# Optimization experiments

Measured on AMD Instinct MI355X. Metric: run time of the kernel, lower is better.

The kernel has to match this reference:

```python
import math
import jax, jax.numpy as jnp
import numpy as np

B, S, D, H = 4, 1024, 512, 8
DH = D // H  # 64
SQRT_DIM = math.sqrt(D)


def _relative_shift(pos_score):
    # pos_score: [B, H, S, S]
    b, h, s1, s2 = pos_score.shape
    zeros = jnp.zeros((b, h, s1, 1), dtype=pos_score.dtype)
    padded = jnp.concatenate([zeros, pos_score], axis=-1)      # [B,H,S,S+1]
    padded = padded.reshape(b, h, s2 + 1, s1)                  # [B,H,S+1,S]
    return padded[:, :, 1:].reshape(b, h, s1, s2)


def setup_inputs() -> dict:
    key = jax.random.key(0)
    ks = jax.random.split(key, 14)
    std = 0.02
    inp = {
        "query": jax.random.normal(ks[0], (B, S, D), jnp.float32),
        "key": jax.random.normal(ks[1], (B, S, D), jnp.float32),
        "value": jax.random.normal(ks[2], (B, S, D), jnp.float32),
        "pos_embedding": jax.random.normal(ks[3], (B, S, D), jnp.float32),
        # projection weights stored [in, out] so y = x @ W + b
        "Wq": jax.random.normal(ks[4], (D, D), jnp.float32) * std,
        "bq": jnp.zeros((D,), jnp.float32),
        "Wk": jax.random.normal(ks[5], (D, D), jnp.float32) * std,
        "bk": jnp.zeros((D,), jnp.float32),
        "Wv": jax.random.normal(ks[6], (D, D), jnp.float32) * std,
        "bv": jnp.zeros((D,), jnp.float32),
        "Wp": jax.random.normal(ks[7], (D, D), jnp.float32) * std,  # pos_proj, no bias
        "Wo": jax.random.normal(ks[8], (D, D), jnp.float32) * std,
        "bo": jnp.zeros((D,), jnp.float32),
        "u_bias": jax.random.normal(ks[9], (H, DH), jnp.float32) * std,
        "v_bias": jax.random.normal(ks[10], (H, DH), jnp.float32) * std,
    }
    return inp


def reference(query, key, value, pos_embedding, Wq, bq, Wk, bk, Wv, bv, Wp, Wo, bo, u_bias, v_bias):
    b = query.shape[0]
    q = (query @ Wq + bq).reshape(b, -1, H, DH)          # [B,S,H,DH]
    k = (key @ Wk + bk).reshape(b, -1, H, DH)            # [B,T,H,DH]
    v = (value @ Wv + bv).reshape(b, -1, H, DH)          # [B,T,H,DH]
    p = (pos_embedding @ Wp).reshape(b, -1, H, DH)       # [B,T,H,DH]

    # content score: (q + u) . k  -> [B,H,S,T]
    content_score = jnp.einsum('bshd,bthd->bhst', q + u_bias, k)
    # position score: (q + v) . pos -> [B,H,S,T], then relative shift
    pos_score = jnp.einsum('bshd,bthd->bhst', q + v_bias, p)
    pos_score = _relative_shift(pos_score)

    score = (content_score + pos_score) / SQRT_DIM
    attn = jax.nn.softmax(score, axis=-1)                # dropout p=0 (eval)

    context = jnp.einsum('bhst,bthd->bshd', attn, v).reshape(b, -1, D)
    out = context @ Wo + bo
    return (out, attn)
```

## Files before the change

### kernel.cpp

```cpp
#include <hip/hip_runtime.h>
#include <hip/hip_bf16.h>

#define B_  4
#define S_  1024
#define D_  512
#define H_  8
#define DH_ 64
#define SCALE 0.044194173824159216f

typedef short bf16x8 __attribute__((ext_vector_type(8)));
typedef float f32x4  __attribute__((ext_vector_type(4)));

__device__ __forceinline__ unsigned short f2bf(float x) {
    union { __hip_bfloat16 h; unsigned short u; } cv;
    cv.h = __float2bfloat16(x);
    return cv.u;
}
__device__ __forceinline__ float bf2f(unsigned short h) {
    union { unsigned int u; float f; } v; v.u = ((unsigned int)h) << 16;
    return v.f;
}

__global__ __launch_bounds__(256) void convert_wt_k(
    const float* __restrict__ W0, const float* __restrict__ W1,
    const float* __restrict__ W2, const float* __restrict__ W3,
    const float* __restrict__ W4,
    unsigned short* __restrict__ T0, unsigned short* __restrict__ T1,
    unsigned short* __restrict__ T2, unsigned short* __restrict__ T3,
    unsigned short* __restrict__ T4)
{
    __shared__ float tile[64][65];
    const float* W;
    unsigned short* T;
    switch (blockIdx.z) {
        case 0: W = W0; T = T0; break;
        case 1: W = W1; T = T1; break;
        case 2: W = W2; T = T2; break;
        case 3: W = W3; T = T3; break;
        default: W = W4; T = T4; break;
    }
    const int r0 = blockIdx.y * 64, c0 = blockIdx.x * 64;
    const int tx = threadIdx.x & 63, ty = threadIdx.x >> 6;
#pragma unroll
    for (int it = 0; it < 16; ++it)
        tile[ty + 4 * it][tx] = W[(size_t)(r0 + ty + 4 * it) * 512 + c0 + tx];
    __syncthreads();
#pragma unroll
    for (int it = 0; it < 16; ++it)
        T[(size_t)(c0 + ty + 4 * it) * 512 + r0 + tx] = f2bf(tile[tx][ty + 4 * it]);
}

__global__ __launch_bounds__(512) void proj_all_k(
    const float* __restrict__ Aq_, const float* __restrict__ Ak_,
    const float* __restrict__ Ap_, const float* __restrict__ Av_,
    const unsigned short* __restrict__ WqT, const unsigned short* __restrict__ WkT,
    const unsigned short* __restrict__ WpT, const unsigned short* __restrict__ WvT,
    const float* __restrict__ bq, const float* __restrict__ bk,
    const float* __restrict__ bv,
    const float* __restrict__ ub, const float* __restrict__ vb,
    unsigned short* __restrict__ qu, unsigned short* __restrict__ qv,
    unsigned short* __restrict__ kbf, unsigned short* __restrict__ pbf,
    unsigned short* __restrict__ v2)
{
    __shared__ unsigned short Ab[128][72];
    __shared__ unsigned short Bb[128][72];
    const int mode = blockIdx.z;
    const float* A;
    const unsigned short* BT;
    switch (mode) {
        case 0: A = Aq_; BT = WqT; break;
        case 1: A = Ak_; BT = WkT; break;
        case 2: A = Ap_; BT = WpT; break;
        default: A = Av_; BT = WvT; break;
    }
    const int tid = threadIdx.x;
    const int i0 = blockIdx.x * 128, j0 = blockIdx.y * 128;
    const int w = tid >> 6, lane = tid & 63, l15 = lane & 15, lhi = lane >> 4;
    const int mr0 = (w >> 1) * 32, nc0 = (w & 1) * 64;
    f32x4 acc[2][4] = {};

    for (int k0 = 0; k0 < 512; k0 += 64) {
        __syncthreads();
#pragma unroll
        for (int it = 0; it < 4; ++it) {
            const int s = tid + it * 512;
            const int row = s >> 4, f4 = (s & 15) * 4;
            float4 va = *(const float4*)&A[(size_t)(i0 + row) * 512 + k0 + f4];
            ushort4 hh;
            hh.x = f2bf(va.x); hh.y = f2bf(va.y); hh.z = f2bf(va.z); hh.w = f2bf(va.w);
            *(ushort4*)&Ab[row][f4] = hh;
        }
#pragma unroll
        for (int it = 0; it < 2; ++it) {
            const int s = tid + it * 512;
            const int row = s >> 3, g = (s & 7) * 8;
            *(bf16x8*)&Bb[row][g] = *(const bf16x8*)&BT[(size_t)(j0 + row) * 512 + k0 + g];
        }
        __syncthreads();
#pragma unroll
        for (int kk = 0; kk < 2; ++kk) {
            bf16x8 a0 = *(const bf16x8*)&Ab[mr0 + l15][kk * 32 + lhi * 8];
            bf16x8 a1 = *(const bf16x8*)&Ab[mr0 + 16 + l15][kk * 32 + lhi * 8];
#pragma unroll
            for (int n = 0; n < 4; ++n) {
                bf16x8 bn = *(const bf16x8*)&Bb[nc0 + 16 * n + l15][kk * 32 + lhi * 8];
                acc[0][n] = __builtin_amdgcn_mfma_f32_16x16x32_bf16(a0, bn, acc[0][n], 0, 0, 0);
                acc[1][n] = __builtin_amdgcn_mfma_f32_16x16x32_bf16(a1, bn, acc[1][n], 0, 0, 0);
            }
        }
    }

#pragma unroll
    for (int m = 0; m < 2; ++m)
#pragma unroll
        for (int n = 0; n < 4; ++n)
#pragma unroll
            for (int r = 0; r < 4; ++r) {
                const int grow = i0 + mr0 + 16 * m + 4 * lhi + r;
                const int gcol = j0 + nc0 + 16 * n + l15;
                const int b = grow >> 10, s = grow & 1023;
                const int h = gcol >> 6, d = gcol & 63;
                const float v = acc[m][n][r];
                if (mode == 3) {
                    const size_t idx = (((size_t)(b * H_ + h) * 32 + (s >> 5)) * 64 + d) * 32 + (s & 31);
                    v2[idx] = f2bf(v + bv[gcol]);
                } else {
                    const size_t idx = (((size_t)b * H_ + h) * S_ + s) * DH_ + d;
                    if (mode == 0) {
                        const float base = v + bq[gcol];
                        qu[idx] = f2bf(base + ub[gcol]);
                        qv[idx] = f2bf(base + vb[gcol]);
                    } else if (mode == 1) {
                        kbf[idx] = f2bf(v + bk[gcol]);
                    } else {
                        pbf[idx] = f2bf(v);
                    }
                }
            }
}

__global__ __launch_bounds__(256) void gemm_bf16_k(
    const unsigned short* __restrict__ A,
    const unsigned short* __restrict__ BT,
    const float* __restrict__ bias,
    float* __restrict__ C)
{
    __shared__ unsigned short Ab[64][72];
    __shared__ unsigned short Bb[64][72];
    const int tid = threadIdx.x;
    const int i0 = blockIdx.x * 64, j0 = blockIdx.y * 64;
    const int w = tid >> 6, lane = tid & 63, l15 = lane & 15, lhi = lane >> 4;
    const int mr0 = (w >> 1) * 32, nc0 = (w & 1) * 32;
    f32x4 acc[2][2] = {};

    for (int k0 = 0; k0 < 512; k0 += 64) {
        __syncthreads();
#pragma unroll
        for (int it = 0; it < 2; ++it) {
            const int s = tid + it * 256;
            const int row = s >> 3, g = (s & 7) * 8;
            *(bf16x8*)&Ab[row][g] = *(const bf16x8*)&A[(size_t)(i0 + row) * 512 + k0 + g];
            *(bf16x8*)&Bb[row][g] = *(const bf16x8*)&BT[(size_t)(j0 + row) * 512 + k0 + g];
        }
        __syncthreads();
#pragma unroll
        for (int kk = 0; kk < 2; ++kk) {
            bf16x8 a0 = *(const bf16x8*)&Ab[mr0 + l15][kk * 32 + lhi * 8];
            bf16x8 a1 = *(const bf16x8*)&Ab[mr0 + 16 + l15][kk * 32 + lhi * 8];
            bf16x8 b0 = *(const bf16x8*)&Bb[nc0 + l15][kk * 32 + lhi * 8];
            bf16x8 b1 = *(const bf16x8*)&Bb[nc0 + 16 + l15][kk * 32 + lhi * 8];
            acc[0][0] = __builtin_amdgcn_mfma_f32_16x16x32_bf16(a0, b0, acc[0][0], 0, 0, 0);
            acc[0][1] = __builtin_amdgcn_mfma_f32_16x16x32_bf16(a0, b1, acc[0][1], 0, 0, 0);
            acc[1][0] = __builtin_amdgcn_mfma_f32_16x16x32_bf16(a1, b0, acc[1][0], 0, 0, 0);
            acc[1][1] = __builtin_amdgcn_mfma_f32_16x16x32_bf16(a1, b1, acc[1][1], 0, 0, 0);
        }
    }

#pragma unroll
    for (int m = 0; m < 2; ++m)
#pragma unroll
        for (int n = 0; n < 2; ++n)
#pragma unroll
            for (int r = 0; r < 4; ++r) {
                const int grow = i0 + mr0 + 16 * m + 4 * lhi + r;
                const int gcol = j0 + nc0 + 16 * n + l15;
                C[(size_t)grow * 512 + gcol] = acc[m][n][r] + bias[gcol];
            }
}

#define RS 1032
#define QBLK 16

__global__ __launch_bounds__(512, 4) void score_fused_k(
    const unsigned short* __restrict__ qu_g,
    const unsigned short* __restrict__ qv_g,
    const unsigned short* __restrict__ kb_g,
    const unsigned short* __restrict__ pb_g,
    const unsigned short* __restrict__ v2_g,
    float* __restrict__ attn,
    unsigned short* __restrict__ ctx_g)
{
    __shared__ unsigned short Sb[128][72];
    __shared__ unsigned short Rsh[16 * RS];
    __shared__ float red[16][9];

    const int tid = threadIdx.x;
    const int i0 = blockIdx.x * QBLK;
    const int bh = blockIdx.y;
    const int w = tid >> 6, lane = tid & 63, l15 = lane & 15, lhi = lane >> 4;

    const unsigned short* qu_b = qu_g + (size_t)bh * S_ * DH_;
    const unsigned short* qv_b = qv_g + (size_t)bh * S_ * DH_;
    const unsigned short* kb_b = kb_g + (size_t)bh * S_ * DH_;
    const unsigned short* pb_b = pb_g + (size_t)bh * S_ * DH_;

    if (tid < 16) {
        const int j = i0 + tid + 1;
        if (j <= 1023) Rsh[tid * RS + j] = 0;
    }

    bf16x8 qf[2], aq0[2], aq1[2];
    {
        const int qrow  = i0 + l15;
        const int qrow1 = min(i0 + 16 + l15, S_ - 1);
#pragma unroll
        for (int kk = 0; kk < 2; ++kk) {
            const int off = kk * 32 + lhi * 8;
            qf[kk]  = *(const bf16x8*)&qu_b[(size_t)qrow  * DH_ + off];
            aq0[kk] = *(const bf16x8*)&qv_b[(size_t)qrow  * DH_ + off];
            aq1[kk] = *(const bf16x8*)&qv_b[(size_t)qrow1 * DH_ + off];
        }
    }

    const int srow0 = 16 * w + (lane >> 3);
    const int sseg  = (lane & 7) * 8;

    bf16x8 kreg[2], preg[2];
#pragma unroll
    for (int it = 0; it < 2; ++it) {
        const size_t g = (size_t)(srow0 + it * 8) * DH_ + sseg;
        kreg[it] = *(const bf16x8*)&kb_b[g];
        preg[it] = *(const bf16x8*)&pb_b[g];
    }

    f32x4 acc[8] = {};
#pragma unroll
    for (int jc = 0; jc < 8; ++jc) {
#pragma unroll
        for (int it = 0; it < 2; ++it)
            *(bf16x8*)&Sb[srow0 + it * 8][sseg] = kreg[it];
        if (jc < 7) {
#pragma unroll
            for (int it = 0; it < 2; ++it) {
                const size_t g = (size_t)((jc + 1) * 128 + srow0 + it * 8) * DH_ + sseg;
                kreg[it] = *(const bf16x8*)&kb_b[g];
            }
        }
        {
            bf16x8 kf0 = *(const bf16x8*)&Sb[16 * w + l15][lhi * 8];
            bf16x8 kf1 = *(const bf16x8*)&Sb[16 * w + l15][32 + lhi * 8];
            acc[jc] = __builtin_amdgcn_mfma_f32_16x16x32_bf16(qf[0], kf0, acc[jc], 0, 0, 0);
            acc[jc] = __builtin_amdgcn_mfma_f32_16x16x32_bf16(qf[1], kf1, acc[jc], 0, 0, 0);
        }
#pragma unroll
        for (int it = 0; it < 2; ++it)
            *(bf16x8*)&Sb[srow0 + it * 8][sseg] = preg[it];
        if (jc < 7) {
#pragma unroll
            for (int it = 0; it < 2; ++it) {
                const size_t g = (size_t)((jc + 1) * 128 + srow0 + it * 8) * DH_ + sseg;
                preg[it] = *(const bf16x8*)&pb_b[g];
            }
        }
        f32x4 racc0 = {}, racc1 = {};
        {
            bf16x8 pf0 = *(const bf16x8*)&Sb[16 * w + l15][lhi * 8];
            bf16x8 pf1 = *(const bf16x8*)&Sb[16 * w + l15][32 + lhi * 8];
            racc0 = __builtin_amdgcn_mfma_f32_16x16x32_bf16(aq0[0], pf0, racc0, 0, 0, 0);
            racc0 = __builtin_amdgcn_mfma_f32_16x16x32_bf16(aq0[1], pf1, racc0, 0, 0, 0);
            racc1 = __builtin_amdgcn_mfma_f32_16x16x32_bf16(aq1[0], pf0, racc1, 0, 0, 0);
            racc1 = __builtin_amdgcn_mfma_f32_16x16x32_bf16(aq1[1], pf1, racc1, 0, 0, 0);
        }

        const int u = jc * 128 + 16 * w + l15;
#pragma unroll
        for (int r = 0; r < 4; ++r) {
            const int rl = 4 * lhi + r;
            const int gr = i0 + rl;
            const int jlo = u + gr - 1023;
            const unsigned short val = f2bf(racc0[r]);
            if (jlo >= 0)      Rsh[rl * RS + jlo] = val;
            else if (rl >= 1)  Rsh[(rl - 1) * RS + (u + gr + 1)] = val;
        }
        if (lhi == 0) {
            const int jhi = u + i0 + 17;
            if (jhi <= 1023) Rsh[15 * RS + jhi] = f2bf(racc1[0]);
        }
    }
    __syncthreads();

    const int b4 = bh >> 3, h4 = bh & 7;
    const int nblk = w & 3;
    const int kh = w >> 2;
    const unsigned short* v2b = v2_g + (size_t)bh * 32 * 2048;
    const int dd = 16 * nblk + l15;
    bf16x8 bbufA[8];
#pragma unroll
    for (int ki = 0; ki < 8; ++ki) {
        const int tb = kh * 16 + ki;
        bbufA[ki] = *(const bf16x8*)&v2b[(size_t)tb * 2048 + dd * 32 + lhi * 8];
    }

    const int il = 4 * lhi;
    float rmax[4], rsum[4];
#pragma unroll
    for (int r = 0; r < 4; ++r) rmax[r] = -3.0e38f;

#pragma unroll
    for (int jc = 0; jc < 8; ++jc)
#pragma unroll
        for (int r = 0; r < 4; ++r) {
            const int row = il + r;
            const int j = jc * 128 + 16 * w + l15;
            const float pos = bf2f(Rsh[row * RS + j]);
            const float s = (acc[jc][r] + pos) * SCALE;
            acc[jc][r] = s;
            rmax[r] = fmaxf(rmax[r], s);
        }

#pragma unroll
    for (int r = 0; r < 4; ++r)
#pragma unroll
        for (int off = 1; off < 16; off <<= 1)
            rmax[r] = fmaxf(rmax[r], __shfl_xor(rmax[r], off));
    if (l15 == 0)
#pragma unroll
        for (int r = 0; r < 4; ++r) red[il + r][w] = rmax[r];
    __syncthreads();
#pragma unroll
    for (int r = 0; r < 4; ++r) {
        float mx = red[il + r][0];
#pragma unroll
        for (int ww = 1; ww < 8; ++ww) mx = fmaxf(mx, red[il + r][ww]);
        rmax[r] = mx;
        rsum[r] = 0.f;
    }
    __syncthreads();

#pragma unroll
    for (int jc = 0; jc < 8; ++jc)
#pragma unroll
        for (int r = 0; r < 4; ++r) {
            const float e = __expf(acc[jc][r] - rmax[r]);
            acc[jc][r] = e;
            rsum[r] += e;
        }
#pragma unroll
    for (int r = 0; r < 4; ++r)
#pragma unroll
        for (int off = 1; off < 16; off <<= 1)
            rsum[r] += __shfl_xor(rsum[r], off);
    if (l15 == 0)
#pragma unroll
        for (int r = 0; r < 4; ++r) red[il + r][w] = rsum[r];
    __syncthreads();

    float* attn_b = attn + (size_t)bh * S_ * S_;
#pragma unroll
    for (int r = 0; r < 4; ++r) {
        float sum = red[il + r][0];
#pragma unroll
        for (int ww = 1; ww < 8; ++ww) sum += red[il + r][ww];
        const float inv = 1.f / sum;
#pragma unroll
        for (int jc = 0; jc < 8; ++jc) {
            const int j = jc * 128 + 16 * w + l15;
            const float pn = acc[jc][r] * inv;
            attn_b[(size_t)(i0 + il + r) * S_ + j] = pn;
            Rsh[(il + r) * RS + j] = f2bf(pn);
        }
    }
    __syncthreads();

    bf16x8 bbufB[8];
#pragma unroll
    for (int ki = 0; ki < 8; ++ki) {
        const int tb = kh * 16 + 8 + ki;
        bbufB[ki] = *(const bf16x8*)&v2b[(size_t)tb * 2048 + dd * 32 + lhi * 8];
    }
    f32x4 cacc = {};
#pragma unroll
    for (int ki = 0; ki < 8; ++ki) {
        const int t0 = (kh * 16 + ki) * 32 + lhi * 8;
        bf16x8 a = *(const bf16x8*)&Rsh[l15 * RS + t0];
        cacc = __builtin_amdgcn_mfma_f32_16x16x32_bf16(a, bbufA[ki], cacc, 0, 0, 0);
    }
#pragma unroll
    for (int ki = 0; ki < 8; ++ki) {
        const int t0 = (kh * 16 + 8 + ki) * 32 + lhi * 8;
        bf16x8 a = *(const bf16x8*)&Rsh[l15 * RS + t0];
        cacc = __builtin_amdgcn_mfma_f32_16x16x32_bf16(a, bbufB[ki], cacc, 0, 0, 0);
    }
    float* fred = (float*)&Sb[0][0];
    if (kh == 0) {
#pragma unroll
        for (int r = 0; r < 4; ++r)
            fred[(nblk * 16 + 4 * lhi + r) * 16 + l15] = cacc[r];
    }
    __syncthreads();
    if (kh == 1) {
#pragma unroll
        for (int r = 0; r < 4; ++r) {
            const float vs = cacc[r] + fred[(nblk * 16 + 4 * lhi + r) * 16 + l15];
            const int srow = i0 + 4 * lhi + r;
            ctx_g[((size_t)(b4 * S_ + srow)) * D_ + h4 * DH_ + 16 * nblk + l15] = f2bf(vs);
        }
    }
}

extern "C" void kernel_launch(void* const* d_in, const int* in_sizes, int n_in,
                              void* d_out, int out_size, void* d_ws, size_t ws_size,
                              hipStream_t stream)
{
    const float* query = (const float*)d_in[0];
    const float* key_  = (const float*)d_in[1];
    const float* value = (const float*)d_in[2];
    const float* pose  = (const float*)d_in[3];
    const float* Wq = (const float*)d_in[4];
    const float* bq = (const float*)d_in[5];
    const float* Wk = (const float*)d_in[6];
    const float* bk = (const float*)d_in[7];
    const float* Wv = (const float*)d_in[8];
    const float* bv = (const float*)d_in[9];
    const float* Wp = (const float*)d_in[10];
    const float* Wo = (const float*)d_in[11];
    const float* bo = (const float*)d_in[12];
    const float* u_bias = (const float*)d_in[13];
    const float* v_bias = (const float*)d_in[14];

    const size_t NTOK = (size_t)B_ * S_ * D_;
    float* out  = (float*)d_out;
    float* attn = (float*)d_out + NTOK;

    unsigned short* qu  = (unsigned short*)d_ws;
    unsigned short* qv  = qu + NTOK;
    unsigned short* kbf = qv + NTOK;
    unsigned short* pbf = kbf + NTOK;
    unsigned short* WqT = pbf + NTOK;
    unsigned short* WkT = WqT + 262144;
    unsigned short* WpT = WkT + 262144;
    unsigned short* WvT = WpT + 262144;
    unsigned short* WoT = WvT + 262144;
    unsigned short* v2  = WoT + 262144;
    unsigned short* ctx = v2 + NTOK;

    const dim3 blk256(256);
    const dim3 gproj(64, 8);

    convert_wt_k<<<dim3(8, 8, 5), blk256, 0, stream>>>(Wq, Wk, Wp, Wv, Wo,
                                                       WqT, WkT, WpT, WvT, WoT);

    proj_all_k<<<dim3(32, 4, 4), dim3(512), 0, stream>>>(
        query, key_, pose, value,
        WqT, WkT, WpT, WvT,
        bq, bk, bv, u_bias, v_bias,
        qu, qv, kbf, pbf, v2);

    score_fused_k<<<dim3(S_ / QBLK, B_ * H_), dim3(512), 0, stream>>>(
        qu, qv, kbf, pbf, v2, attn, ctx);

    gemm_bf16_k<<<gproj, blk256, 0, stream>>>(ctx, WoT, bo, out);
}
```

Measured before the change: 113.5 us.

## Store K and P projections in MFMA fragment order and load directly to registers

```diff
diff --git a/kernel.cpp b/kernel.cpp
--- a/kernel.cpp
+++ b/kernel.cpp
@@ -124,17 +124,18 @@
                 if (mode == 3) {
                     const size_t idx = (((size_t)(b * H_ + h) * 32 + (s >> 5)) * 64 + d) * 32 + (s & 31);
                     v2[idx] = f2bf(v + bv[gcol]);
+                } else if (mode == 0) {
+                    const size_t idx = (((size_t)b * H_ + h) * S_ + s) * DH_ + d;
+                    const float base = v + bq[gcol];
+                    qu[idx] = f2bf(base + ub[gcol]);
+                    qv[idx] = f2bf(base + vb[gcol]);
                 } else {
-                    const size_t idx = (((size_t)b * H_ + h) * S_ + s) * DH_ + d;
-                    if (mode == 0) {
-                        const float base = v + bq[gcol];
-                        qu[idx] = f2bf(base + ub[gcol]);
-                        qv[idx] = f2bf(base + vb[gcol]);
-                    } else if (mode == 1) {
-                        kbf[idx] = f2bf(v + bk[gcol]);
-                    } else {
-                        pbf[idx] = f2bf(v);
-                    }
+                    const int jc = s >> 7, wch = (s >> 4) & 7, l15o = s & 15;
+                    const int kko = d >> 5, lhio = (d >> 3) & 3, dso = d & 7;
+                    const size_t idx = (size_t)(b * H_ + h) * 65536
+                        + (size_t)(((jc * 2 + kko) * 8 + wch) * 64 + lhio * 16 + l15o) * 8 + dso;
+                    if (mode == 1) kbf[idx] = f2bf(v + bk[gcol]);
+                    else           pbf[idx] = f2bf(v);
                 }
             }
 }
@@ -200,9 +201,9 @@
     float* __restrict__ attn,
     unsigned short* __restrict__ ctx_g)
 {
-    __shared__ unsigned short Sb[128][72];
     __shared__ unsigned short Rsh[16 * RS];
     __shared__ float red[16][9];
+    __shared__ float fred[1024];
 
     const int tid = threadIdx.x;
     const int i0 = blockIdx.x * QBLK;
@@ -211,8 +212,8 @@
 
     const unsigned short* qu_b = qu_g + (size_t)bh * S_ * DH_;
     const unsigned short* qv_b = qv_g + (size_t)bh * S_ * DH_;
-    const unsigned short* kb_b = kb_g + (size_t)bh * S_ * DH_;
-    const unsigned short* pb_b = pb_g + (size_t)bh * S_ * DH_;
+    const unsigned short* kb_b = kb_g + (size_t)bh * 65536;
+    const unsigned short* pb_b = pb_g + (size_t)bh * 65536;
 
     if (tid < 16) {
         const int j = i0 + tid + 1;
@@ -232,55 +233,23 @@
         }
     }
 
-    const int srow0 = 16 * w + (lane >> 3);
-    const int sseg  = (lane & 7) * 8;
-
-    bf16x8 kreg[2], preg[2];
-#pragma unroll
-    for (int it = 0; it < 2; ++it) {
-        const size_t g = (size_t)(srow0 + it * 8) * DH_ + sseg;
-        kreg[it] = *(const bf16x8*)&kb_b[g];
-        preg[it] = *(const bf16x8*)&pb_b[g];
-    }
-
+    const size_t lbase = (size_t)w * 512 + (size_t)lane * 8;
     f32x4 acc[8] = {};
 #pragma unroll
     for (int jc = 0; jc < 8; ++jc) {
-#pragma unroll
-        for (int it = 0; it < 2; ++it)
-            *(bf16x8*)&Sb[srow0 + it * 8][sseg] = kreg[it];
-        if (jc < 7) {
-#pragma unroll
-            for (int it = 0; it < 2; ++it) {
-                const size_t g = (size_t)((jc + 1) * 128 + srow0 + it * 8) * DH_ + sseg;
-                kreg[it] = *(const bf16x8*)&kb_b[g];
-            }
-        }
-        {
-            bf16x8 kf0 = *(const bf16x8*)&Sb[16 * w + l15][lhi * 8];
-            bf16x8 kf1 = *(const bf16x8*)&Sb[16 * w + l15][32 + lhi * 8];
-            acc[jc] = __builtin_amdgcn_mfma_f32_16x16x32_bf16(qf[0], kf0, acc[jc], 0, 0, 0);
-            acc[jc] = __builtin_amdgcn_mfma_f32_16x16x32_bf16(qf[1], kf1, acc[jc], 0, 0, 0);
-        }
-#pragma unroll
-        for (int it = 0; it < 2; ++it)
-            *(bf16x8*)&Sb[srow0 + it * 8][sseg] = preg[it];
-        if (jc < 7) {
-#pragma unroll
-            for (int it = 0; it < 2; ++it) {
-                const size_t g = (size_t)((jc + 1) * 128 + srow0 + it * 8) * DH_ + sseg;
-                preg[it] = *(const bf16x8*)&pb_b[g];
-            }
-        }
+        const size_t cb = (size_t)jc * 8192 + lbase;
+        bf16x8 kf0 = *(const bf16x8*)&kb_b[cb];
+        bf16x8 kf1 = *(const bf16x8*)&kb_b[cb + 4096];
+        bf16x8 pf0 = *(const bf16x8*)&pb_b[cb];
+        bf16x8 pf1 = *(const bf16x8*)&pb_b[cb + 4096];
+
+        acc[jc] = __builtin_amdgcn_mfma_f32_16x16x32_bf16(qf[0], kf0, acc[jc], 0, 0, 0);
+        acc[jc] = __builtin_amdgcn_mfma_f32_16x16x32_bf16(qf[1], kf1, acc[jc], 0, 0, 0);
         f32x4 racc0 = {}, racc1 = {};
-        {
-            bf16x8 pf0 = *(const bf16x8*)&Sb[16 * w + l15][lhi * 8];
-            bf16x8 pf1 = *(const bf16x8*)&Sb[16 * w + l15][32 + lhi * 8];
-            racc0 = __builtin_amdgcn_mfma_f32_16x16x32_bf16(aq0[0], pf0, racc0, 0, 0, 0);
-            racc0 = __builtin_amdgcn_mfma_f32_16x16x32_bf16(aq0[1], pf1, racc0, 0, 0, 0);
-            racc1 = __builtin_amdgcn_mfma_f32_16x16x32_bf16(aq1[0], pf0, racc1, 0, 0, 0);
-            racc1 = __builtin_amdgcn_mfma_f32_16x16x32_bf16(aq1[1], pf1, racc1, 0, 0, 0);
-        }
+        racc0 = __builtin_amdgcn_mfma_f32_16x16x32_bf16(aq0[0], pf0, racc0, 0, 0, 0);
+        racc0 = __builtin_amdgcn_mfma_f32_16x16x32_bf16(aq0[1], pf1, racc0, 0, 0, 0);
+        racc1 = __builtin_amdgcn_mfma_f32_16x16x32_bf16(aq1[0], pf0, racc1, 0, 0, 0);
+        racc1 = __builtin_amdgcn_mfma_f32_16x16x32_bf16(aq1[1], pf1, racc1, 0, 0, 0);
 
         const int u = jc * 128 + 16 * w + l15;
 #pragma unroll
@@ -401,7 +370,6 @@
         bf16x8 a = *(const bf16x8*)&Rsh[l15 * RS + t0];
         cacc = __builtin_amdgcn_mfma_f32_16x16x32_bf16(a, bbufB[ki], cacc, 0, 0, 0);
     }
-    float* fred = (float*)&Sb[0][0];
     if (kh == 0) {
 #pragma unroll
         for (int r = 0; r < 4; ++r)
```

After: 117.4 us. +3.5%, slower.
